# Kernel optimization log

Hardware: AMD Instinct MI355X
Metric: run time of the kernel (lower is better)

## Reference

```python
import jax, jax.numpy as jnp
import numpy as np

F_DIM = 128


def setup_inputs() -> dict:
    key = jax.random.key(0)
    ks = jax.random.split(key, 10)
    n_atoms = 50000
    n_edges = 500000
    F = F_DIM
    q = jax.random.normal(ks[0], (n_atoms, 1, F), dtype=jnp.float32)
    mu = jax.random.normal(ks[1], (n_atoms, 3, F), dtype=jnp.float32)
    Wij = jax.random.normal(ks[2], (n_edges, 1, 3 * F), dtype=jnp.float32)
    dir_ij = jax.random.normal(ks[3], (n_edges, 3), dtype=jnp.float32)
    idx_i = jax.random.randint(ks[4], (n_edges,), 0, n_atoms, dtype=jnp.int32)
    idx_j = jax.random.randint(ks[5], (n_edges,), 0, n_atoms, dtype=jnp.int32)
    # interatomic_context_net params: Dense(F,F,silu) -> Dense(F,3F)
    s1 = 1.0 / np.sqrt(F)
    W1 = jax.random.uniform(ks[6], (F, F), jnp.float32, -s1, s1)
    b1 = jax.random.uniform(ks[7], (F,), jnp.float32, -s1, s1)
    W2 = jax.random.uniform(ks[8], (F, 3 * F), jnp.float32, -s1, s1)
    b2 = jax.random.uniform(ks[9], (3 * F,), jnp.float32, -s1, s1)
    return {"q": q, "mu": mu, "Wij": Wij, "dir_ij": dir_ij,
            "W1": W1, "b1": b1, "W2": W2, "b2": b2,
            "idx_i": idx_i, "idx_j": idx_j, "n_atoms": n_atoms}


def reference(q, mu, Wij, dir_ij, W1, b1, W2, b2, idx_i, idx_j, n_atoms):
    F = F_DIM
    # context MLP on per-atom scalar features: [n_atoms, 1, 3F]
    h = jax.nn.silu(jnp.einsum('aif,fg->aig', q, W1) + b1)
    x = jnp.einsum('aif,fg->aig', h, W2) + b2
    # gather along edges
    xj = x[idx_j]          # [E, 1, 3F]
    muj = mu[idx_j]        # [E, 3, F]
    xw = Wij * xj          # [E, 1, 3F]
    dq, dmuR, dmumu = jnp.split(xw, 3, axis=-1)  # each [E, 1, F]
    dq_atom = jax.ops.segment_sum(dq, idx_i, num_segments=n_atoms)  # [n_atoms,1,F]
    dmu = dmuR * dir_ij[..., None] + dmumu * muj                    # [E,3,F]
    dmu_atom = jax.ops.segment_sum(dmu, idx_i, num_segments=n_atoms)
    return (q + dq_atom, mu + dmu_atom)
```

## Files before the change

kernel.cpp:

```cpp
#include <hip/hip_runtime.h>

typedef unsigned short u16;
typedef unsigned int   u32;
typedef unsigned long long u64;

#define F 128
#define F3 384
#define TA 32
#define PAD 36
#define ROW 768

__device__ __forceinline__ float bf2f(u16 v) {
    union { u32 u; float f; } c; c.u = ((u32)v) << 16; return c.f;
}
__device__ __forceinline__ u16 f2bf(float f) {
    union { float fv; u32 u; } c; c.fv = f;
    u32 u = c.u;
    return (u16)((u + 0x7fffu + ((u >> 16) & 1u)) >> 16);
}
__device__ __forceinline__ float u2f(u32 v) {
    union { u32 u; float f; } c; c.u = v; return c.f;
}
__device__ __forceinline__ u32 f2u(float v) {
    union { float f; u32 u; } c; c.f = v; return c.u;
}
__device__ __forceinline__ u32 pk(float a, float b) {
    return ((u32)f2bf(b) << 16) | f2bf(a);
}

template<bool BF> __device__ __forceinline__ float LD(const void* p, size_t i) {
    return BF ? bf2f(((const u16*)p)[i]) : ((const float*)p)[i];
}
template<bool BF> __device__ __forceinline__ float2 LD2(const void* p, size_t i) {
    if (BF) {
        u32 v = *(const u32*)((const u16*)p + i);
        float2 r; r.x = bf2f((u16)(v & 0xffff)); r.y = bf2f((u16)(v >> 16)); return r;
    }
    return *(const float2*)((const float*)p + i);
}
template<bool BF> __device__ __forceinline__ void ST2(void* p, size_t i, float2 v) {
    if (BF) { *(u32*)((u16*)p + i) = pk(v.x, v.y); }
    else    { *(float2*)((float*)p + i) = v; }
}
__device__ __forceinline__ float2 LD2bf(const u16* p, size_t i) {
    u32 v = *(const u32*)(p + i);
    float2 r; r.x = bf2f((u16)(v & 0xffff)); r.y = bf2f((u16)(v >> 16)); return r;
}
template<bool BF> __device__ __forceinline__ float4 LD4(const void* p, size_t i) {
    if (BF) {
        uint2 v = *(const uint2*)((const u16*)p + i);
        float4 r;
        r.x = bf2f((u16)(v.x & 0xffff)); r.y = bf2f((u16)(v.x >> 16));
        r.z = bf2f((u16)(v.y & 0xffff)); r.w = bf2f((u16)(v.y >> 16));
        return r;
    }
    return *(const float4*)((const float*)p + i);
}
template<bool BF> __device__ __forceinline__ float2 NTLD2(const void* p, size_t i) {
    if (BF) {
        u32 v = __builtin_nontemporal_load((const u32*)((const u16*)p + i));
        float2 r; r.x = bf2f((u16)(v & 0xffff)); r.y = bf2f((u16)(v >> 16)); return r;
    } else {
        u64 v = __builtin_nontemporal_load((const u64*)((const float*)p + i));
        float2 r; r.x = u2f((u32)v); r.y = u2f((u32)(v >> 32)); return r;
    }
}
template<bool BF> __device__ __forceinline__ void NTST2(void* p, size_t i, float2 v) {
    if (BF) {
        u32 o = pk(v.x, v.y);
        __builtin_nontemporal_store(o, (u32*)((u16*)p + i));
    } else {
        u64 o = ((u64)f2u(v.y) << 32) | f2u(v.x);
        __builtin_nontemporal_store(o, (u64*)((float*)p + i));
    }
}

__global__ __launch_bounds__(256) void detect_kernel(const void* q, int* flag) {
    __shared__ int cnt;
    if (threadIdx.x == 0) cnt = 0;
    __syncthreads();
    const u16* p = (const u16*)q;
    int c = 0;
    for (int i = threadIdx.x; i < 1024; i += 256) {
        u16 v = p[2 * i];
        int e = (v >> 7) & 0xFF;
        if (e >= 100 && e <= 150) c++;
    }
    atomicAdd(&cnt, c);
    __syncthreads();
    if (threadIdx.x == 0) *flag = (cnt > 512) ? 1 : 0;
}

template<bool BF>
__device__ void mu12_body(const void* mu, u16* xm12, int n_atoms) {
    int a = blockIdx.x * 4 + (threadIdx.x >> 6);
    int p = threadIdx.x & 63;
    if (a >= n_atoms) return;
    float2 m0 = LD2<BF>(mu, (size_t)a * F3 + 2 * p);
    float2 m1 = LD2<BF>(mu, (size_t)a * F3 + 128 + 2 * p);
    float2 m2 = LD2<BF>(mu, (size_t)a * F3 + 256 + 2 * p);
    u16* base = xm12 + (size_t)a * ROW + p * 12;
    *(u32*)(base + 6) = pk(m0.x, m0.y);
    *(uint2*)(base + 8) = make_uint2(pk(m1.x, m1.y), pk(m2.x, m2.y));
}
__global__ __launch_bounds__(256) void mu12_kernel(const void* mu, u16* xm12,
                                                   int n_atoms, const int* flag) {
    if (*flag) mu12_body<true >(mu, xm12, n_atoms);
    else       mu12_body<false>(mu, xm12, n_atoms);
}

template<bool BF>
__device__ void mlpfull_body(const void* q, const void* W1, const void* b1,
                             const void* W2, const void* b2,
                             u16* __restrict__ xm12, int n_atoms)
{
    __shared__ float qT[F][PAD];
    __shared__ float hT[F][PAD];

    const int tid = threadIdx.x;
    const int a0  = blockIdx.x * TA;
    const int c4  = (tid & 31) * 4;
    const int r4  = (tid >> 5) * 4;

    for (int i = tid; i < TA * F / 8; i += 256) {
        int a = i >> 4, f0 = (i & 15) * 8;
        float4 v0, v1;
        if (a0 + a < n_atoms) {
            v0 = LD4<BF>(q, (size_t)(a0 + a) * F + f0);
            v1 = LD4<BF>(q, (size_t)(a0 + a) * F + f0 + 4);
        } else { v0 = v1 = make_float4(0, 0, 0, 0); }
        qT[f0 + 0][a] = v0.x; qT[f0 + 1][a] = v0.y; qT[f0 + 2][a] = v0.z; qT[f0 + 3][a] = v0.w;
        qT[f0 + 4][a] = v1.x; qT[f0 + 5][a] = v1.y; qT[f0 + 6][a] = v1.z; qT[f0 + 7][a] = v1.w;
    }
    __syncthreads();

    {
        float acc[4][4];
#pragma unroll
        for (int rr = 0; rr < 4; ++rr)
#pragma unroll
            for (int cc = 0; cc < 4; ++cc) acc[rr][cc] = 0.0f;

        for (int f = 0; f < F; ++f) {
            float4 qv = *(const float4*)&qT[f][r4];
            float4 w  = LD4<BF>(W1, (size_t)f * F + c4);
            float qa[4] = {qv.x, qv.y, qv.z, qv.w};
            float wa[4] = {w.x, w.y, w.z, w.w};
#pragma unroll
            for (int rr = 0; rr < 4; ++rr)
#pragma unroll
                for (int cc = 0; cc < 4; ++cc)
                    acc[rr][cc] += qa[rr] * wa[cc];
        }
#pragma unroll
        for (int cc = 0; cc < 4; ++cc) {
            float bb = LD<BF>(b1, c4 + cc);
#pragma unroll
            for (int rr = 0; rr < 4; ++rr) {
                float h = acc[rr][cc] + bb;
                hT[c4 + cc][r4 + rr] = h / (1.0f + __expf(-h));
            }
        }
    }
    __syncthreads();

    float xout[4][4][3];
#pragma unroll
    for (int cb = 0; cb < 3; ++cb) {
        float acc[4][4];
#pragma unroll
        for (int rr = 0; rr < 4; ++rr)
#pragma unroll
            for (int cc = 0; cc < 4; ++cc) acc[rr][cc] = 0.0f;

        for (int f = 0; f < F; ++f) {
            float4 hv = *(const float4*)&hT[f][r4];
            float4 w  = LD4<BF>(W2, (size_t)f * F3 + cb * F + c4);
            float ha[4] = {hv.x, hv.y, hv.z, hv.w};
            float wa[4] = {w.x, w.y, w.z, w.w};
#pragma unroll
            for (int rr = 0; rr < 4; ++rr)
#pragma unroll
                for (int cc = 0; cc < 4; ++cc)
                    acc[rr][cc] += ha[rr] * wa[cc];
        }
#pragma unroll
        for (int cc = 0; cc < 4; ++cc) {
            float bb = LD<BF>(b2, cb * F + c4 + cc);
#pragma unroll
            for (int rr = 0; rr < 4; ++rr)
                xout[rr][cc][cb] = acc[rr][cc] + bb;
        }
    }
#pragma unroll
    for (int rr = 0; rr < 4; ++rr) {
        int ga = a0 + r4 + rr;
        if (ga < n_atoms) {
            int p0 = c4 >> 1;
            u16* b0 = xm12 + (size_t)ga * ROW + p0 * 12;
            *(uint2*)(b0) = make_uint2(pk(xout[rr][0][0], xout[rr][1][0]),
                                       pk(xout[rr][0][1], xout[rr][1][1]));
            *(u32*)(b0 + 4) = pk(xout[rr][0][2], xout[rr][1][2]);
            u16* b1p = b0 + 12;
            *(uint2*)(b1p) = make_uint2(pk(xout[rr][2][0], xout[rr][3][0]),
                                        pk(xout[rr][2][1], xout[rr][3][1]));
            *(u32*)(b1p + 4) = pk(xout[rr][2][2], xout[rr][3][2]);
        }
    }
}
__global__ __launch_bounds__(256) void mlpfull_kernel(
    const void* q, const void* W1, const void* b1, const void* W2, const void* b2,
    u16* xm12, int n_atoms, const int* flag)
{
    if (*flag) mlpfull_body<true >(q, W1, b1, W2, b2, xm12, n_atoms);
    else       mlpfull_body<false>(q, W1, b1, W2, b2, xm12, n_atoms);
}

__global__ __launch_bounds__(256) void count_kernel(
    const int* __restrict__ idx_i, int* __restrict__ counts, int E)
{
    int e = blockIdx.x * 256 + threadIdx.x;
    if (e < E) atomicAdd(&counts[idx_i[e]], 1);
}

__global__ __launch_bounds__(1024) void scan_kernel(
    const int* __restrict__ counts, int* __restrict__ offsets, int n)
{
    __shared__ int buf[1024];
    const int t = threadIdx.x;
    const int m = (n + 1023) >> 10;
    const int i0 = t * m;
    int s = 0;
    for (int r = 0; r < m; ++r) {
        int i = i0 + r;
        if (i < n) s += counts[i];
    }
    buf[t] = s;
    __syncthreads();
    for (int off = 1; off < 1024; off <<= 1) {
        int add = (t >= off) ? buf[t - off] : 0;
        __syncthreads();
        buf[t] += add;
        __syncthreads();
    }
    int run = buf[t] - s;
    for (int r = 0; r < m; ++r) {
        int i = i0 + r;
        if (i < n) { offsets[i] = run; run += counts[i]; }
    }
    if (t == 1023) offsets[n] = buf[1023];
}

template<bool BF>
__device__ void scatter_body(const int* __restrict__ idx_i, const int* __restrict__ idx_j,
                             const void* __restrict__ dir, const int* __restrict__ offsets,
                             int* __restrict__ cursor, int4* __restrict__ ej4, int E)
{
    int e = blockIdx.x * 256 + threadIdx.x;
    if (e < E) {
        int i = idx_i[e];
        int pos = offsets[i] + atomicAdd(&cursor[i], 1);
        float d0 = LD<BF>(dir, (size_t)e * 3 + 0);
        float d1 = LD<BF>(dir, (size_t)e * 3 + 1);
        float d2 = LD<BF>(dir, (size_t)e * 3 + 2);
        int4 v;
        v.x = e;
        v.y = idx_j[e];
        v.z = (int)pk(d0, d1);
        v.w = (int)(u32)f2bf(d2);
        ej4[pos] = v;
    }
}
__global__ __launch_bounds__(256) void scatter_kernel(
    const int* idx_i, const int* idx_j, const void* dir, const int* offsets,
    int* cursor, int4* ej4, int E, const int* flag)
{
    if (*flag) scatter_body<true >(idx_i, idx_j, dir, offsets, cursor, ej4, E);
    else       scatter_body<false>(idx_i, idx_j, dir, offsets, cursor, ej4, E);
}

template<bool BF>
__device__ void gfused_body(const void* q, const void* mu, const void* Wij,
                            const u16* __restrict__ xm12,
                            const int4* __restrict__ ej4,
                            const int* __restrict__ offsets,
                            void* out, int n_atoms, int E)
{
    int a    = blockIdx.x * 4 + (threadIdx.x >> 6);
    int lane = threadIdx.x & 63;
    if (a >= n_atoms) return;
    const size_t fo = 2 * lane;
    const size_t ob = (size_t)n_atoms * F;

    float2 sq = LD2<BF>(q, (size_t)a * F + fo);
    float2 s0 = LD2<BF>(mu, (size_t)a * F3 + fo);
    float2 s1 = LD2<BF>(mu, (size_t)a * F3 + 128 + fo);
    float2 s2 = LD2<BF>(mu, (size_t)a * F3 + 256 + fo);

    int k0 = offsets[a], k1 = offsets[a + 1];
    for (int kb = k0; kb < k1; kb += 64) {
        int cnt = k1 - kb; if (cnt > 64) cnt = 64;
        int e_r = 0, j_r = 0, d01_r = 0, d2_r = 0;
        if (lane < cnt) {
            int4 t = ej4[kb + lane];
            e_r = t.x; if ((unsigned)e_r >= (unsigned)E) e_r = 0;
            j_r = t.y; if ((unsigned)j_r >= (unsigned)n_atoms) j_r = 0;
            d01_r = t.z; d2_r = t.w;
        }
#pragma unroll 4
        for (int c = 0; c < cnt; ++c) {
            int e   = __shfl(e_r, c, 64);
            int j   = __shfl(j_r, c, 64);
            int d01 = __shfl(d01_r, c, 64);
            int d2i = __shfl(d2_r, c, 64);
            float d0 = bf2f((u16)((u32)d01 & 0xffff));
            float d1 = bf2f((u16)((u32)d01 >> 16));
            float d2 = bf2f((u16)((u32)d2i & 0xffff));

            float2 wq = NTLD2<BF>(Wij, (size_t)e * F3 + fo);
            float2 wR = NTLD2<BF>(Wij, (size_t)e * F3 + 128 + fo);
            float2 wm = NTLD2<BF>(Wij, (size_t)e * F3 + 256 + fo);

            const u16* row = xm12 + (size_t)j * ROW + lane * 12;
            uint2 v0 = *(const uint2*)(row);
            uint2 v1 = *(const uint2*)(row + 4);
            uint2 v2 = *(const uint2*)(row + 8);

            float xq0 = bf2f((u16)(v0.x & 0xffff)), xq1 = bf2f((u16)(v0.x >> 16));
            float xR0 = bf2f((u16)(v0.y & 0xffff)), xR1 = bf2f((u16)(v0.y >> 16));
            float xm0 = bf2f((u16)(v1.x & 0xffff)), xm1 = bf2f((u16)(v1.x >> 16));
            float m00 = bf2f((u16)(v1.y & 0xffff)), m01 = bf2f((u16)(v1.y >> 16));
            float m10 = bf2f((u16)(v2.x & 0xffff)), m11 = bf2f((u16)(v2.x >> 16));
            float m20 = bf2f((u16)(v2.y & 0xffff)), m21 = bf2f((u16)(v2.y >> 16));

            sq.x += wq.x * xq0;  sq.y += wq.y * xq1;
            float tR0 = wR.x * xR0, tR1 = wR.y * xR1;
            float tm0 = wm.x * xm0, tm1 = wm.y * xm1;
            s0.x += tR0 * d0 + tm0 * m00;  s0.y += tR1 * d0 + tm1 * m01;
            s1.x += tR0 * d1 + tm0 * m10;  s1.y += tR1 * d1 + tm1 * m11;
            s2.x += tR0 * d2 + tm0 * m20;  s2.y += tR1 * d2 + tm1 * m21;
        }
    }
    NTST2<BF>(out, (size_t)a * F + fo, sq);
    NTST2<BF>(out, ob + (size_t)a * F3 + fo,       s0);
    NTST2<BF>(out, ob + (size_t)a * F3 + 128 + fo, s1);
    NTST2<BF>(out, ob + (size_t)a * F3 + 256 + fo, s2);
}
__global__ __launch_bounds__(256) void gfused_kernel(
    const void* q, const void* mu, const void* Wij,
    const u16* xm12, const int4* ej4, const int* offsets,
    void* out, int n_atoms, int E, const int* flag)
{
    if (*flag) gfused_body<true >(q, mu, Wij, xm12, ej4, offsets, out, n_atoms, E);
    else       gfused_body<false>(q, mu, Wij, xm12, ej4, offsets, out, n_atoms, E);
}

extern "C" void kernel_launch(void* const* d_in, const int* in_sizes, int n_in,
                              void* d_out, int out_size, void* d_ws, size_t ws_size,
                              hipStream_t stream)
{
    const void* q   = d_in[0];
    const void* mu  = d_in[1];
    const void* Wij = d_in[2];
    const void* dir = d_in[3];
    const void* W1  = d_in[4];
    const void* b1  = d_in[5];
    const void* W2  = d_in[6];
    const void* b2  = d_in[7];
    const int* idx_i = (const int*)d_in[8];
    const int* idx_j = (const int*)d_in[9];

    const int n_atoms = in_sizes[0] / F;
    const int E       = in_sizes[8];
    const int eBlocks   = (E + 255) / 256;
    const int gBlocks   = (n_atoms + 3) / 4;
    const int mlpBlocks = (n_atoms + TA - 1) / TA;

    u16*  xm12    = (u16*)d_ws;
    int*  flag    = (int*)(xm12 + (size_t)n_atoms * ROW);
    int*  counts  = flag + 4;
    int*  cursor  = counts + n_atoms;
    int*  offsets = cursor + n_atoms;
    int4* ej4     = (int4*)(((size_t)(offsets + n_atoms + 1) + 15) & ~(size_t)15);

    detect_kernel<<<1, 256, 0, stream>>>(q, flag);
    hipMemsetAsync(counts, 0, (size_t)2 * n_atoms * sizeof(int), stream);
    count_kernel<<<eBlocks, 256, 0, stream>>>(idx_i, counts, E);
    scan_kernel<<<1, 1024, 0, stream>>>(counts, offsets, n_atoms);
    scatter_kernel<<<eBlocks, 256, 0, stream>>>(idx_i, idx_j, dir, offsets,
                                                cursor, ej4, E, flag);

    mu12_kernel<<<gBlocks, 256, 0, stream>>>(mu, xm12, n_atoms, flag);
    mlpfull_kernel<<<mlpBlocks, 256, 0, stream>>>(q, W1, b1, W2, b2, xm12, n_atoms, flag);

    gfused_kernel<<<gBlocks, 256, 0, stream>>>(q, mu, Wij, xm12, ej4, offsets,
                                               d_out, n_atoms, E, flag);
}
```

Before: 586.1 us.

## Pre-sort edge weights into bf16 CSR order during scatter

The scatter kernel now uses one wavefront per edge. Each wavefront copies that edge's Wij row, converted to bf16, into a workspace buffer ordered by the destination-sorted position. The fused gather kernel then streams these weights contiguously instead of gathering by edge id. This trades an extra full read and write of the weight tensor for sequential, half-size weight reads in the main kernel, and quantizes fp32 weights to bf16.

```diff
diff --git a/kernel.cpp b/kernel.cpp
--- a/kernel.cpp
+++ b/kernel.cpp
@@ -41,10 +41,6 @@
 template<bool BF> __device__ __forceinline__ void ST2(void* p, size_t i, float2 v) {
     if (BF) { *(u32*)((u16*)p + i) = pk(v.x, v.y); }
     else    { *(float2*)((float*)p + i) = v; }
-}
-__device__ __forceinline__ float2 LD2bf(const u16* p, size_t i) {
-    u32 v = *(const u32*)(p + i);
-    float2 r; r.x = bf2f((u16)(v & 0xffff)); r.y = bf2f((u16)(v >> 16)); return r;
 }
 template<bool BF> __device__ __forceinline__ float4 LD4(const void* p, size_t i) {
     if (BF) {
@@ -55,15 +51,6 @@
         return r;
     }
     return *(const float4*)((const float*)p + i);
-}
-template<bool BF> __device__ __forceinline__ float2 NTLD2(const void* p, size_t i) {
-    if (BF) {
-        u32 v = __builtin_nontemporal_load((const u32*)((const u16*)p + i));
-        float2 r; r.x = bf2f((u16)(v & 0xffff)); r.y = bf2f((u16)(v >> 16)); return r;
-    } else {
-        u64 v = __builtin_nontemporal_load((const u64*)((const float*)p + i));
-        float2 r; r.x = u2f((u32)v); r.y = u2f((u32)(v >> 32)); return r;
-    }
 }
 template<bool BF> __device__ __forceinline__ void NTST2(void* p, size_t i, float2 v) {
     if (BF) {
@@ -252,14 +239,19 @@
 }
 
 template<bool BF>
-__device__ void scatter_body(const int* __restrict__ idx_i, const int* __restrict__ idx_j,
-                             const void* __restrict__ dir, const int* __restrict__ offsets,
-                             int* __restrict__ cursor, int4* __restrict__ ej4, int E)
-{
-    int e = blockIdx.x * 256 + threadIdx.x;
-    if (e < E) {
+__device__ void scatter_w_body(const int* __restrict__ idx_i, const int* __restrict__ idx_j,
+                               const void* __restrict__ dir, const void* __restrict__ Wij,
+                               const int* __restrict__ offsets, int* __restrict__ cursor,
+                               int4* __restrict__ ej4, u16* __restrict__ wbf, int E)
+{
+    int e    = blockIdx.x * 4 + (threadIdx.x >> 6);
+    int lane = threadIdx.x & 63;
+    if (e >= E) return;
+
+    int pos = 0;
+    if (lane == 0) {
         int i = idx_i[e];
-        int pos = offsets[i] + atomicAdd(&cursor[i], 1);
+        pos = offsets[i] + atomicAdd(&cursor[i], 1);
         float d0 = LD<BF>(dir, (size_t)e * 3 + 0);
         float d1 = LD<BF>(dir, (size_t)e * 3 + 1);
         float d2 = LD<BF>(dir, (size_t)e * 3 + 2);
@@ -270,17 +262,28 @@
         v.w = (int)(u32)f2bf(d2);
         ej4[pos] = v;
     }
-}
-__global__ __launch_bounds__(256) void scatter_kernel(
-    const int* idx_i, const int* idx_j, const void* dir, const int* offsets,
-    int* cursor, int4* ej4, int E, const int* flag)
-{
-    if (*flag) scatter_body<true >(idx_i, idx_j, dir, offsets, cursor, ej4, E);
-    else       scatter_body<false>(idx_i, idx_j, dir, offsets, cursor, ej4, E);
+    pos = __shfl(pos, 0, 64);
+
+    const size_t fo = 2 * (size_t)lane;
+    float2 wq = LD2<BF>(Wij, (size_t)e * F3 + fo);
+    float2 wR = LD2<BF>(Wij, (size_t)e * F3 + 128 + fo);
+    float2 wm = LD2<BF>(Wij, (size_t)e * F3 + 256 + fo);
+    u16* row = wbf + (size_t)pos * F3;
+    *(u32*)(row + fo)       = pk(wq.x, wq.y);
+    *(u32*)(row + 128 + fo) = pk(wR.x, wR.y);
+    *(u32*)(row + 256 + fo) = pk(wm.x, wm.y);
+}
+__global__ __launch_bounds__(256) void scatter_w_kernel(
+    const int* idx_i, const int* idx_j, const void* dir, const void* Wij,
+    const int* offsets, int* cursor, int4* ej4, u16* wbf, int E, const int* flag)
+{
+    if (*flag) scatter_w_body<true >(idx_i, idx_j, dir, Wij, offsets, cursor, ej4, wbf, E);
+    else       scatter_w_body<false>(idx_i, idx_j, dir, Wij, offsets, cursor, ej4, wbf, E);
 }
 
 template<bool BF>
-__device__ void gfused_body(const void* q, const void* mu, const void* Wij,
+__device__ void gfused_body(const void* q, const void* mu,
+                            const u16* __restrict__ wbf,
                             const u16* __restrict__ xm12,
                             const int4* __restrict__ ej4,
                             const int* __restrict__ offsets,
@@ -300,16 +303,14 @@
     int k0 = offsets[a], k1 = offsets[a + 1];
     for (int kb = k0; kb < k1; kb += 64) {
         int cnt = k1 - kb; if (cnt > 64) cnt = 64;
-        int e_r = 0, j_r = 0, d01_r = 0, d2_r = 0;
+        int j_r = 0, d01_r = 0, d2_r = 0;
         if (lane < cnt) {
             int4 t = ej4[kb + lane];
-            e_r = t.x; if ((unsigned)e_r >= (unsigned)E) e_r = 0;
             j_r = t.y; if ((unsigned)j_r >= (unsigned)n_atoms) j_r = 0;
             d01_r = t.z; d2_r = t.w;
         }
 #pragma unroll 4
         for (int c = 0; c < cnt; ++c) {
-            int e   = __shfl(e_r, c, 64);
             int j   = __shfl(j_r, c, 64);
             int d01 = __shfl(d01_r, c, 64);
             int d2i = __shfl(d2_r, c, 64);
@@ -317,14 +318,19 @@
             float d1 = bf2f((u16)((u32)d01 >> 16));
             float d2 = bf2f((u16)((u32)d2i & 0xffff));
 
-            float2 wq = NTLD2<BF>(Wij, (size_t)e * F3 + fo);
-            float2 wR = NTLD2<BF>(Wij, (size_t)e * F3 + 128 + fo);
-            float2 wm = NTLD2<BF>(Wij, (size_t)e * F3 + 256 + fo);
+            const u16* wrow = wbf + (size_t)(kb + c) * F3;
+            u32 wqv = __builtin_nontemporal_load((const u32*)(wrow + fo));
+            u32 wRv = __builtin_nontemporal_load((const u32*)(wrow + 128 + fo));
+            u32 wmv = __builtin_nontemporal_load((const u32*)(wrow + 256 + fo));
 
             const u16* row = xm12 + (size_t)j * ROW + lane * 12;
             uint2 v0 = *(const uint2*)(row);
             uint2 v1 = *(const uint2*)(row + 4);
             uint2 v2 = *(const uint2*)(row + 8);
+
+            float wq0 = bf2f((u16)(wqv & 0xffff)), wq1 = bf2f((u16)(wqv >> 16));
+            float wR0 = bf2f((u16)(wRv & 0xffff)), wR1 = bf2f((u16)(wRv >> 16));
+            float wm0 = bf2f((u16)(wmv & 0xffff)), wm1 = bf2f((u16)(wmv >> 16));
 
             float xq0 = bf2f((u16)(v0.x & 0xffff)), xq1 = bf2f((u16)(v0.x >> 16));
             float xR0 = bf2f((u16)(v0.y & 0xffff)), xR1 = bf2f((u16)(v0.y >> 16));
@@ -333,9 +339,9 @@
             float m10 = bf2f((u16)(v2.x & 0xffff)), m11 = bf2f((u16)(v2.x >> 16));
             float m20 = bf2f((u16)(v2.y & 0xffff)), m21 = bf2f((u16)(v2.y >> 16));
 
-            sq.x += wq.x * xq0;  sq.y += wq.y * xq1;
-            float tR0 = wR.x * xR0, tR1 = wR.y * xR1;
-            float tm0 = wm.x * xm0, tm1 = wm.y * xm1;
+            sq.x += wq0 * xq0;  sq.y += wq1 * xq1;
+            float tR0 = wR0 * xR0, tR1 = wR1 * xR1;
+            float tm0 = wm0 * xm0, tm1 = wm1 * xm1;
             s0.x += tR0 * d0 + tm0 * m00;  s0.y += tR1 * d0 + tm1 * m01;
             s1.x += tR0 * d1 + tm0 * m10;  s1.y += tR1 * d1 + tm1 * m11;
             s2.x += tR0 * d2 + tm0 * m20;  s2.y += tR1 * d2 + tm1 * m21;
@@ -347,12 +353,12 @@
     NTST2<BF>(out, ob + (size_t)a * F3 + 256 + fo, s2);
 }
 __global__ __launch_bounds__(256) void gfused_kernel(
-    const void* q, const void* mu, const void* Wij,
+    const void* q, const void* mu, const u16* wbf,
     const u16* xm12, const int4* ej4, const int* offsets,
     void* out, int n_atoms, int E, const int* flag)
 {
-    if (*flag) gfused_body<true >(q, mu, Wij, xm12, ej4, offsets, out, n_atoms, E);
-    else       gfused_body<false>(q, mu, Wij, xm12, ej4, offsets, out, n_atoms, E);
+    if (*flag) gfused_body<true >(q, mu, wbf, xm12, ej4, offsets, out, n_atoms, E);
+    else       gfused_body<false>(q, mu, wbf, xm12, ej4, offsets, out, n_atoms, E);
 }
 
 extern "C" void kernel_launch(void* const* d_in, const int* in_sizes, int n_in,
@@ -373,10 +379,12 @@
     const int n_atoms = in_sizes[0] / F;
     const int E       = in_sizes[8];
     const int eBlocks   = (E + 255) / 256;
+    const int ewBlocks  = (E + 3) / 4;
     const int gBlocks   = (n_atoms + 3) / 4;
     const int mlpBlocks = (n_atoms + TA - 1) / TA;
 
-    u16*  xm12    = (u16*)d_ws;
+    u16*  wbf     = (u16*)d_ws;
+    u16*  xm12    = wbf + (size_t)E * F3;
     int*  flag    = (int*)(xm12 + (size_t)n_atoms * ROW);
     int*  counts  = flag + 4;
     int*  cursor  = counts + n_atoms;
@@ -387,12 +395,12 @@
     hipMemsetAsync(counts, 0, (size_t)2 * n_atoms * sizeof(int), stream);
     count_kernel<<<eBlocks, 256, 0, stream>>>(idx_i, counts, E);
     scan_kernel<<<1, 1024, 0, stream>>>(counts, offsets, n_atoms);
-    scatter_kernel<<<eBlocks, 256, 0, stream>>>(idx_i, idx_j, dir, offsets,
-                                                cursor, ej4, E, flag);
+    scatter_w_kernel<<<ewBlocks, 256, 0, stream>>>(idx_i, idx_j, dir, Wij, offsets,
+                                                   cursor, ej4, wbf, E, flag);
 
     mu12_kernel<<<gBlocks, 256, 0, stream>>>(mu, xm12, n_atoms, flag);
     mlpfull_kernel<<<mlpBlocks, 256, 0, stream>>>(q, W1, b1, W2, b2, xm12, n_atoms, flag);
 
-    gfused_kernel<<<gBlocks, 256, 0, stream>>>(q, mu, Wij, xm12, ej4, offsets,
+    gfused_kernel<<<gBlocks, 256, 0, stream>>>(q, mu, wbf, xm12, ej4, offsets,
                                                d_out, n_atoms, E, flag);
 }
```

Measured after the change: 801.1 us. 1.37x slower.

## Compute context MLP with bf16 MFMA instead of scalar FP32 FMA

Applied to the files above, without the earlier changes.

Rewrites the per-atom two-layer MLP kernel to stage q and transposed weights in shared memory as bf16 and use 16x16x32 bf16 MFMA instructions for both matmuls. This is meant to remove the scalar FP32 FMA cost of the atom-side GEMMs. In exchange, each block re-transposes W1 and all W2 slices into LDS, the MLP inputs are rounded to bf16, and outputs are written as scattered 2-byte stores.

```diff
diff --git a/kernel.cpp b/kernel.cpp
--- a/kernel.cpp
+++ b/kernel.cpp
@@ -6,9 +6,11 @@
 
 #define F 128
 #define F3 384
-#define TA 32
-#define PAD 36
 #define ROW 768
+#define KP 136
+
+typedef __attribute__((ext_vector_type(8))) short bf16x8;
+typedef __attribute__((ext_vector_type(4))) float f32x4;
 
 __device__ __forceinline__ float bf2f(u16 v) {
     union { u32 u; float f; } c; c.u = ((u32)v) << 16; return c.f;
@@ -37,14 +39,6 @@
         float2 r; r.x = bf2f((u16)(v & 0xffff)); r.y = bf2f((u16)(v >> 16)); return r;
     }
     return *(const float2*)((const float*)p + i);
-}
-template<bool BF> __device__ __forceinline__ void ST2(void* p, size_t i, float2 v) {
-    if (BF) { *(u32*)((u16*)p + i) = pk(v.x, v.y); }
-    else    { *(float2*)((float*)p + i) = v; }
-}
-__device__ __forceinline__ float2 LD2bf(const u16* p, size_t i) {
-    u32 v = *(const u32*)(p + i);
-    float2 r; r.x = bf2f((u16)(v & 0xffff)); r.y = bf2f((u16)(v >> 16)); return r;
 }
 template<bool BF> __device__ __forceinline__ float4 LD4(const void* p, size_t i) {
     if (BF) {
@@ -56,6 +50,15 @@
     }
     return *(const float4*)((const float*)p + i);
 }
+template<bool BF> __device__ __forceinline__ void NTST2(void* p, size_t i, float2 v) {
+    if (BF) {
+        u32 o = pk(v.x, v.y);
+        __builtin_nontemporal_store(o, (u32*)((u16*)p + i));
+    } else {
+        u64 o = ((u64)f2u(v.y) << 32) | f2u(v.x);
+        __builtin_nontemporal_store(o, (u64*)((float*)p + i));
+    }
+}
 template<bool BF> __device__ __forceinline__ float2 NTLD2(const void* p, size_t i) {
     if (BF) {
         u32 v = __builtin_nontemporal_load((const u32*)((const u16*)p + i));
@@ -63,15 +66,6 @@
     } else {
         u64 v = __builtin_nontemporal_load((const u64*)((const float*)p + i));
         float2 r; r.x = u2f((u32)v); r.y = u2f((u32)(v >> 32)); return r;
-    }
-}
-template<bool BF> __device__ __forceinline__ void NTST2(void* p, size_t i, float2 v) {
-    if (BF) {
-        u32 o = pk(v.x, v.y);
-        __builtin_nontemporal_store(o, (u32*)((u16*)p + i));
-    } else {
-        u64 o = ((u64)f2u(v.y) << 32) | f2u(v.x);
-        __builtin_nontemporal_store(o, (u64*)((float*)p + i));
     }
 }
 
@@ -114,98 +108,94 @@
                              const void* W2, const void* b2,
                              u16* __restrict__ xm12, int n_atoms)
 {
-    __shared__ float qT[F][PAD];
-    __shared__ float hT[F][PAD];
-
-    const int tid = threadIdx.x;
-    const int a0  = blockIdx.x * TA;
-    const int c4  = (tid & 31) * 4;
-    const int r4  = (tid >> 5) * 4;
-
-    for (int i = tid; i < TA * F / 8; i += 256) {
-        int a = i >> 4, f0 = (i & 15) * 8;
-        float4 v0, v1;
-        if (a0 + a < n_atoms) {
-            v0 = LD4<BF>(q, (size_t)(a0 + a) * F + f0);
-            v1 = LD4<BF>(q, (size_t)(a0 + a) * F + f0 + 4);
-        } else { v0 = v1 = make_float4(0, 0, 0, 0); }
-        qT[f0 + 0][a] = v0.x; qT[f0 + 1][a] = v0.y; qT[f0 + 2][a] = v0.z; qT[f0 + 3][a] = v0.w;
-        qT[f0 + 4][a] = v1.x; qT[f0 + 5][a] = v1.y; qT[f0 + 6][a] = v1.z; qT[f0 + 7][a] = v1.w;
-    }
-    __syncthreads();
-
-    {
-        float acc[4][4];
-#pragma unroll
-        for (int rr = 0; rr < 4; ++rr)
-#pragma unroll
-            for (int cc = 0; cc < 4; ++cc) acc[rr][cc] = 0.0f;
-
-        for (int f = 0; f < F; ++f) {
-            float4 qv = *(const float4*)&qT[f][r4];
-            float4 w  = LD4<BF>(W1, (size_t)f * F + c4);
-            float qa[4] = {qv.x, qv.y, qv.z, qv.w};
-            float wa[4] = {w.x, w.y, w.z, w.w};
-#pragma unroll
-            for (int rr = 0; rr < 4; ++rr)
-#pragma unroll
-                for (int cc = 0; cc < 4; ++cc)
-                    acc[rr][cc] += qa[rr] * wa[cc];
-        }
-#pragma unroll
-        for (int cc = 0; cc < 4; ++cc) {
-            float bb = LD<BF>(b1, c4 + cc);
-#pragma unroll
-            for (int rr = 0; rr < 4; ++rr) {
-                float h = acc[rr][cc] + bb;
-                hT[c4 + cc][r4 + rr] = h / (1.0f + __expf(-h));
+    __shared__ u16 qbf[32][KP];
+    __shared__ u16 wT [128][KP];
+    __shared__ u16 hbf[32][KP];
+
+    const int tid  = threadIdx.x;
+    const int a0   = blockIdx.x * 32;
+    const int wv   = tid >> 6;
+    const int lane = tid & 63;
+    const int lr   = lane & 15;
+    const int lg   = lane >> 4;
+    const int rowt = wv & 1;
+    const int cbase= (wv >> 1) * 4;
+
+    for (int i = tid; i < 32 * 32; i += 256) {
+        int a = i >> 5, k4 = (i & 31) * 4;
+        float4 v = (a0 + a < n_atoms) ? LD4<BF>(q, (size_t)(a0 + a) * F + k4)
+                                      : make_float4(0, 0, 0, 0);
+        *(uint2*)&qbf[a][k4] = make_uint2(pk(v.x, v.y), pk(v.z, v.w));
+    }
+    for (int i = tid; i < 128 * 32; i += 256) {
+        int col = i & 127, k4 = (i >> 7) * 4;
+        float v0 = LD<BF>(W1, (size_t)(k4 + 0) * F + col);
+        float v1 = LD<BF>(W1, (size_t)(k4 + 1) * F + col);
+        float v2 = LD<BF>(W1, (size_t)(k4 + 2) * F + col);
+        float v3 = LD<BF>(W1, (size_t)(k4 + 3) * F + col);
+        *(uint2*)&wT[col][k4] = make_uint2(pk(v0, v1), pk(v2, v3));
+    }
+    __syncthreads();
+
+    bf16x8 af[4];
+#pragma unroll
+    for (int kk = 0; kk < 4; ++kk)
+        af[kk] = *(const bf16x8*)&qbf[rowt * 16 + lr][kk * 32 + lg * 8];
+
+#pragma unroll
+    for (int ct = 0; ct < 4; ++ct) {
+        int colt = cbase + ct;
+        f32x4 acc = {0.0f, 0.0f, 0.0f, 0.0f};
+#pragma unroll
+        for (int kk = 0; kk < 4; ++kk) {
+            bf16x8 bv = *(const bf16x8*)&wT[colt * 16 + lr][kk * 32 + lg * 8];
+            acc = __builtin_amdgcn_mfma_f32_16x16x32_bf16(af[kk], bv, acc, 0, 0, 0);
+        }
+        int col = colt * 16 + lr;
+        float bb = LD<BF>(b1, col);
+#pragma unroll
+        for (int r = 0; r < 4; ++r) {
+            float h = acc[r] + bb;
+            float s = h / (1.0f + __expf(-h));
+            hbf[rowt * 16 + lg * 4 + r][col] = f2bf(s);
+        }
+    }
+    __syncthreads();
+
+#pragma unroll
+    for (int kk = 0; kk < 4; ++kk)
+        af[kk] = *(const bf16x8*)&hbf[rowt * 16 + lr][kk * 32 + lg * 8];
+
+    for (int cb = 0; cb < 3; ++cb) {
+        for (int i = tid; i < 128 * 32; i += 256) {
+            int col = i & 127, k4 = (i >> 7) * 4;
+            float v0 = LD<BF>(W2, (size_t)(k4 + 0) * F3 + cb * 128 + col);
+            float v1 = LD<BF>(W2, (size_t)(k4 + 1) * F3 + cb * 128 + col);
+            float v2 = LD<BF>(W2, (size_t)(k4 + 2) * F3 + cb * 128 + col);
+            float v3 = LD<BF>(W2, (size_t)(k4 + 3) * F3 + cb * 128 + col);
+            *(uint2*)&wT[col][k4] = make_uint2(pk(v0, v1), pk(v2, v3));
+        }
+        __syncthreads();
+#pragma unroll
+        for (int ct = 0; ct < 4; ++ct) {
+            int colt = cbase + ct;
+            f32x4 acc = {0.0f, 0.0f, 0.0f, 0.0f};
+#pragma unroll
+            for (int kk = 0; kk < 4; ++kk) {
+                bf16x8 bv = *(const bf16x8*)&wT[colt * 16 + lr][kk * 32 + lg * 8];
+                acc = __builtin_amdgcn_mfma_f32_16x16x32_bf16(af[kk], bv, acc, 0, 0, 0);
             }
-        }
-    }
-    __syncthreads();
-
-    float xout[4][4][3];
-#pragma unroll
-    for (int cb = 0; cb < 3; ++cb) {
-        float acc[4][4];
-#pragma unroll
-        for (int rr = 0; rr < 4; ++rr)
-#pragma unroll
-            for (int cc = 0; cc < 4; ++cc) acc[rr][cc] = 0.0f;
-
-        for (int f = 0; f < F; ++f) {
-            float4 hv = *(const float4*)&hT[f][r4];
-            float4 w  = LD4<BF>(W2, (size_t)f * F3 + cb * F + c4);
-            float ha[4] = {hv.x, hv.y, hv.z, hv.w};
-            float wa[4] = {w.x, w.y, w.z, w.w};
-#pragma unroll
-            for (int rr = 0; rr < 4; ++rr)
-#pragma unroll
-                for (int cc = 0; cc < 4; ++cc)
-                    acc[rr][cc] += ha[rr] * wa[cc];
-        }
-#pragma unroll
-        for (int cc = 0; cc < 4; ++cc) {
-            float bb = LD<BF>(b2, cb * F + c4 + cc);
-#pragma unroll
-            for (int rr = 0; rr < 4; ++rr)
-                xout[rr][cc][cb] = acc[rr][cc] + bb;
-        }
-    }
-#pragma unroll
-    for (int rr = 0; rr < 4; ++rr) {
-        int ga = a0 + r4 + rr;
-        if (ga < n_atoms) {
-            int p0 = c4 >> 1;
-            u16* b0 = xm12 + (size_t)ga * ROW + p0 * 12;
-            *(uint2*)(b0) = make_uint2(pk(xout[rr][0][0], xout[rr][1][0]),
-                                       pk(xout[rr][0][1], xout[rr][1][1]));
-            *(u32*)(b0 + 4) = pk(xout[rr][0][2], xout[rr][1][2]);
-            u16* b1p = b0 + 12;
-            *(uint2*)(b1p) = make_uint2(pk(xout[rr][2][0], xout[rr][3][0]),
-                                        pk(xout[rr][2][1], xout[rr][3][1]));
-            *(u32*)(b1p + 4) = pk(xout[rr][2][2], xout[rr][3][2]);
-        }
+            int f = colt * 16 + lr;
+            float bb = LD<BF>(b2, cb * 128 + f);
+#pragma unroll
+            for (int r = 0; r < 4; ++r) {
+                int ga = a0 + rowt * 16 + lg * 4 + r;
+                if (ga < n_atoms)
+                    xm12[(size_t)ga * ROW + (f >> 1) * 12 + (f & 1) + 2 * cb]
+                        = f2bf(acc[r] + bb);
+            }
+        }
+        __syncthreads();
     }
 }
 __global__ __launch_bounds__(256) void mlpfull_kernel(
@@ -374,7 +364,7 @@
     const int E       = in_sizes[8];
     const int eBlocks   = (E + 255) / 256;
     const int gBlocks   = (n_atoms + 3) / 4;
-    const int mlpBlocks = (n_atoms + TA - 1) / TA;
+    const int mlpBlocks = (n_atoms + 31) / 32;
 
     u16*  xm12    = (u16*)d_ws;
     int*  flag    = (int*)(xm12 + (size_t)n_atoms * ROW);
```

After: 556.9 us. -5.0%, faster.
